# Optimization experiments

Hardware: AMD Instinct MI355X
Metric: run time of the kernel (lower is better)

## Reference

```python
import jax, jax.numpy as jnp
import numpy as np

B, C, H, W = 32, 512, 32, 32
C8 = C // 8


def setup_inputs() -> dict:
    key = jax.random.key(0)
    ks = jax.random.split(key, 4)
    x = jax.random.normal(ks[0], (B, C, W, H), dtype=jnp.float32)
    # 1x1 conv weights == channel-mixing matrices [out_c, in_c]
    Wq = jax.random.normal(ks[1], (C8, C), dtype=jnp.float32) * (1.0 / np.sqrt(C))
    Wk = jax.random.normal(ks[2], (C8, C), dtype=jnp.float32) * (1.0 / np.sqrt(C))
    Wv = jax.random.normal(ks[3], (C, C), dtype=jnp.float32) * (1.0 / np.sqrt(C))
    bq = jnp.zeros((C8,), jnp.float32)
    bk = jnp.zeros((C8,), jnp.float32)
    bv = jnp.zeros((C,), jnp.float32)
    alpha = jnp.float32(1.0)  # nonzero so attention path is exercised
    return {"x": x, "Wq": Wq, "bq": bq, "Wk": Wk, "bk": bk, "Wv": Wv, "bv": bv, "alpha": alpha}


def reference(x, Wq, bq, Wk, bk, Wv, bv, alpha):
    b, c, w, h = x.shape
    n = w * h
    xf = x.reshape(b, c, n)  # [B, C, N]
    # 1x1 convs = per-pixel channel GEMMs
    q = jnp.einsum('oc,bcn->bon', Wq, xf) + bq[None, :, None]  # [B, C8, N]
    k = jnp.einsum('oc,bcn->bon', Wk, xf) + bk[None, :, None]  # [B, C8, N]
    v = jnp.einsum('oc,bcn->bon', Wv, xf) + bv[None, :, None]  # [B, C,  N]
    # energy[b, n, m] = q[:, n] . k[:, m]  (unscaled, full attention)
    energy = jnp.einsum('bcn,bcm->bnm', q, k)  # [B, N, N]
    attention = jax.nn.softmax(energy, axis=-1)
    # out[b, c, n] = sum_m v[b, c, m] * attention[b, n, m]
    out = jnp.einsum('bcm,bnm->bcn', v, attention)
    out = out.reshape(b, c, w, h)
    return alpha * out + x
```

## Files before the change

kernel.cpp:

```cpp
#include <hip/hip_runtime.h>
#include <math.h>

#define B_DIM  32
#define C_DIM  512
#define N_DIM  1024
#define LOG2E  1.44269504088896340736f
#define NEG_BIG (-1.0e30f)

typedef __attribute__((ext_vector_type(8))) __bf16 bf16x8;
typedef __attribute__((ext_vector_type(8))) short short8v;
typedef __attribute__((ext_vector_type(4))) short short4v;
typedef __attribute__((ext_vector_type(4))) float floatx4;

__device__ __forceinline__ unsigned short f2bf(float f) {
    unsigned u = __float_as_uint(f);
    return (unsigned short)((u + 0x7FFFu + ((u >> 16) & 1u)) >> 16);
}
__device__ __forceinline__ float bf2f(unsigned short h) {
    return __uint_as_float(((unsigned)h) << 16);
}
__device__ __forceinline__ floatx4 mfma16(short8v a, short8v b, floatx4 c) {
    return __builtin_amdgcn_mfma_f32_16x16x32_bf16(
        __builtin_bit_cast(bf16x8, a), __builtin_bit_cast(bf16x8, b), c, 0, 0, 0);
}
__device__ __forceinline__ float fin(float v) {
    return (__builtin_fabsf(v) <= 1.0e30f) ? v : 0.0f;
}

#define BAR_LDS()  do {                                            \
    asm volatile("s_waitcnt lgkmcnt(0)" ::: "memory");             \
    __builtin_amdgcn_s_barrier();                                  \
    asm volatile("" ::: "memory");                                 \
} while (0)

__global__ __launch_bounds__(256) void tx2_kernel(
    const float* __restrict__ x,
    unsigned short* __restrict__ xth, unsigned short* __restrict__ xtl)
{
    __shared__ float tile[64][65];
    const int n0 = blockIdx.x * 64, c0 = blockIdx.y * 64, b = blockIdx.z;
    const int t = threadIdx.x;

    #pragma unroll
    for (int p = 0; p < 4; ++p) {
        const int r = (t >> 4) + 16 * p;
        const float4 v = *(const float4*)(x + ((size_t)b*C_DIM + c0 + r)*N_DIM
                                          + n0 + (t & 15)*4);
        tile[r][(t&15)*4+0] = v.x;  tile[r][(t&15)*4+1] = v.y;
        tile[r][(t&15)*4+2] = v.z;  tile[r][(t&15)*4+3] = v.w;
    }
    __syncthreads();
    #pragma unroll
    for (int p = 0; p < 2; ++p) {
        const int rn = (t >> 3) + 32 * p;
        const int c8 = (t & 7) * 8;
        short8v hi, lo;
        #pragma unroll
        for (int j = 0; j < 8; ++j) {
            const float f = tile[c8 + j][rn];
            const unsigned short h = f2bf(f);
            hi[j] = (short)h;
            lo[j] = (short)f2bf(f - bf2f(h));
        }
        const size_t base = ((size_t)b*N_DIM + n0 + rn)*C_DIM + c0 + c8;
        *(short8v*)(xth + base) = hi;
        *(short8v*)(xtl + base) = lo;
    }
}

__global__ __launch_bounds__(256) void qkproj_mfma(
    const unsigned short* __restrict__ xth, const unsigned short* __restrict__ xtl,
    const float* __restrict__ Wq, const float* __restrict__ bq,
    const float* __restrict__ Wk, const float* __restrict__ bk,
    unsigned short* __restrict__ qkt)
{
    __shared__ unsigned short Ah[128][40], Al[128][40];
    __shared__ unsigned short Bh[128][40], Bl[128][40];
    const int b = blockIdx.z, n0 = blockIdx.x * 128;
    const int t = threadIdx.x, w = t >> 6, l = t & 63;
    const int la = l & 15, lb = l >> 4;
    const int nh = (w & 1) * 64, oh = (w >> 1) * 64;

    floatx4 acc[4][4];
    #pragma unroll
    for (int i = 0; i < 4; ++i)
        #pragma unroll
        for (int j = 0; j < 4; ++j) acc[i][j] = (floatx4)0.0f;

    for (int k0 = 0; k0 < C_DIM; k0 += 32) {
        #pragma unroll
        for (int p = 0; p < 2; ++p) {
            const int idx = t + 256*p, row = idx >> 2, ch = idx & 3;
            const size_t g = ((size_t)b*N_DIM + n0 + row)*C_DIM + k0 + ch*8;
            *(short8v*)&Ah[row][ch*8] = *(const short8v*)(xth + g);
            *(short8v*)&Al[row][ch*8] = *(const short8v*)(xtl + g);
        }
        #pragma unroll
        for (int p = 0; p < 4; ++p) {
            const int idx = t + 256*p, row = idx >> 3, ch = idx & 7;
            const float* Wrow = (row < 64) ? (Wq + (size_t)row * C_DIM)
                                           : (Wk + (size_t)(row - 64) * C_DIM);
            const float4 wv = *(const float4*)(Wrow + k0 + ch*4);
            const float fv[4] = {wv.x, wv.y, wv.z, wv.w};
            short4v sh, sl;
            #pragma unroll
            for (int j = 0; j < 4; ++j) {
                const unsigned short h = f2bf(fv[j]);
                sh[j] = (short)h;
                sl[j] = (short)f2bf(fv[j] - bf2f(h));
            }
            *(short4v*)&Bh[row][ch*4] = sh;
            *(short4v*)&Bl[row][ch*4] = sl;
        }
        __syncthreads();

        short8v ahf[4], alf[4], bhf[4], blf[4];
        #pragma unroll
        for (int nt = 0; nt < 4; ++nt) {
            ahf[nt] = *(const short8v*)&Ah[nh + nt*16 + la][lb*8];
            alf[nt] = *(const short8v*)&Al[nh + nt*16 + la][lb*8];
        }
        #pragma unroll
        for (int ot = 0; ot < 4; ++ot) {
            bhf[ot] = *(const short8v*)&Bh[oh + ot*16 + la][lb*8];
            blf[ot] = *(const short8v*)&Bl[oh + ot*16 + la][lb*8];
        }
        #pragma unroll
        for (int nt = 0; nt < 4; ++nt)
            #pragma unroll
            for (int ot = 0; ot < 4; ++ot) {
                acc[nt][ot] = mfma16(ahf[nt], bhf[ot], acc[nt][ot]);
                acc[nt][ot] = mfma16(ahf[nt], blf[ot], acc[nt][ot]);
                acc[nt][ot] = mfma16(alf[nt], bhf[ot], acc[nt][ot]);
            }
        __syncthreads();
    }

    const int plane = (oh == 0) ? 0 : 2;
    #pragma unroll
    for (int ot = 0; ot < 4; ++ot) {
        const int o = oh + ot*16 + la;
        const int c = o & 63;
        const float bias = (oh == 0) ? bq[o] : bk[o - 64];
        #pragma unroll
        for (int nt = 0; nt < 4; ++nt)
            #pragma unroll
            for (int r = 0; r < 4; ++r) {
                const int n = n0 + nh + nt*16 + lb*4 + r;
                const float f = acc[nt][ot][r] + bias;
                const unsigned short h = f2bf(f);
                const unsigned short lo16 = f2bf(f - bf2f(h));
                qkt[(((size_t)b*4 + plane    )*N_DIM + n)*64 + c] = h;
                qkt[(((size_t)b*4 + plane + 1)*N_DIM + n)*64 + c] = lo16;
            }
    }
}

__global__ __launch_bounds__(256) void vproj_mfma(
    const unsigned short* __restrict__ xt,
    const float* __restrict__ Wv, const float* __restrict__ bvv,
    unsigned short* __restrict__ vbf)
{
    __shared__ unsigned short Axs[128][40];
    __shared__ unsigned short Bws[128][40];
    const int b = blockIdx.z, m0 = blockIdx.x * 128, c0 = blockIdx.y * 128;
    const int t = threadIdx.x, w = t >> 6, l = t & 63;
    const int la = l & 15, lb = l >> 4;
    const int mh = (w & 1) * 64, chh = (w >> 1) * 64;

    floatx4 acc[4][4];
    #pragma unroll
    for (int i = 0; i < 4; ++i)
        #pragma unroll
        for (int j = 0; j < 4; ++j) acc[i][j] = (floatx4)0.0f;

    for (int k0 = 0; k0 < C_DIM; k0 += 32) {
        #pragma unroll
        for (int p = 0; p < 2; ++p) {
            const int idx = t + 256 * p;
            const int row = idx >> 2, ch = idx & 3;
            *(short8v*)&Axs[row][ch*8] =
                *(const short8v*)(xt + ((size_t)b*N_DIM + m0 + row)*C_DIM + k0 + ch*8);
        }
        #pragma unroll
        for (int p = 0; p < 4; ++p) {
            const int idx = t + 256 * p;
            const int row = idx >> 3, ch = idx & 7;
            const float4 wv = *(const float4*)(Wv + (size_t)(c0 + row)*C_DIM + k0 + ch*4);
            short4v s;
            s[0] = (short)f2bf(wv.x); s[1] = (short)f2bf(wv.y);
            s[2] = (short)f2bf(wv.z); s[3] = (short)f2bf(wv.w);
            *(short4v*)&Bws[row][ch*4] = s;
        }
        __syncthreads();
        short8v af[4], bfv[4];
        #pragma unroll
        for (int mt = 0; mt < 4; ++mt)
            af[mt] = *(const short8v*)&Axs[mh + mt*16 + la][lb*8];
        #pragma unroll
        for (int ct = 0; ct < 4; ++ct)
            bfv[ct] = *(const short8v*)&Bws[chh + ct*16 + la][lb*8];
        #pragma unroll
        for (int mt = 0; mt < 4; ++mt)
            #pragma unroll
            for (int ct = 0; ct < 4; ++ct)
                acc[mt][ct] = mfma16(af[mt], bfv[ct], acc[mt][ct]);
        __syncthreads();
    }
    #pragma unroll
    for (int ct = 0; ct < 4; ++ct) {
        const int c = c0 + chh + ct*16 + la;
        const float bias = bvv[c];
        #pragma unroll
        for (int mt = 0; mt < 4; ++mt) {
            const int m = m0 + mh + mt*16 + lb*4;
            short4v s;
            #pragma unroll
            for (int r = 0; r < 4; ++r) s[r] = (short)f2bf(acc[mt][ct][r] + bias);
            *(short4v*)(vbf + ((size_t)b*C_DIM + c)*N_DIM + m) = s;
        }
    }
}

__global__ __launch_bounds__(256, 2) void attn_mfma(
    const unsigned short* __restrict__ qkt,
    const unsigned short* __restrict__ vbf,
    const float* __restrict__ x,
    const float* __restrict__ alpha_p,
    float* __restrict__ out)
{
    __shared__ unsigned short Qh[32][72], Ql[32][72];
    __shared__ unsigned short Kh[64][72], Kl[64][72];
    __shared__ __align__(16) float S[32][68];
    __shared__ unsigned short Pb[32][72];
    __shared__ float row_m[32], row_l[32], row_scale[32];

    const int id  = blockIdx.x;
    const int lin = (id & 7) * 128 + (id >> 3);
    const int b   = lin >> 5;
    const int n0  = (lin & 31) * 32;

    const int t = threadIdx.x, w = t >> 6, l = t & 63;
    const int la = l & 15, lb = l >> 4;
    const unsigned short* qkb = qkt + (size_t)b * 4 * N_DIM * 64;

    #pragma unroll
    for (int plane = 0; plane < 2; ++plane) {
        const int row = t >> 3;
        const int ch  = t & 7;
        const short8v g = *(const short8v*)(qkb + ((size_t)plane*N_DIM + n0 + row)*64 + ch*8);
        if (plane == 0) *(short8v*)&Qh[row][ch*8] = g;
        else            *(short8v*)&Ql[row][ch*8] = g;
    }
    #pragma unroll
    for (int pp = 0; pp < 4; ++pp) {
        const int plane = pp >> 1;
        const int idx   = t + 256 * (pp & 1);
        const int row   = idx >> 3;
        const int ch    = idx & 7;
        const short8v g = *(const short8v*)(qkb + ((size_t)(2 + plane)*N_DIM + row)*64 + ch*8);
        if (plane == 0) *(short8v*)&Kh[row][ch*8] = g;
        else            *(short8v*)&Kl[row][ch*8] = g;
    }
    if (t < 32) { row_m[t] = NEG_BIG; row_l[t] = 0.0f; row_scale[t] = 1.0f; }
    __syncthreads();

    floatx4 acc[2][8];
    #pragma unroll
    for (int i = 0; i < 2; ++i)
        #pragma unroll
        for (int j = 0; j < 8; ++j) acc[i][j] = (floatx4)0.0f;

    #pragma unroll 1
    for (int it = 0; it < 16; ++it) {
        const int m0  = it * 64;
        const int m0n = (it < 15) ? (m0 + 64) : 0;

        short8v vreg[2][8];
        #pragma unroll
        for (int ks = 0; ks < 2; ++ks) {
            const unsigned short* vp =
                vbf + ((size_t)b*C_DIM + w*128 + la)*N_DIM + m0 + ks*32 + lb*8;
            #pragma unroll
            for (int ct = 0; ct < 8; ++ct)
                vreg[ks][ct] = *(const short8v*)(vp + (size_t)ct*16*N_DIM);
        }
        short8v kreg[4];
        #pragma unroll
        for (int pp = 0; pp < 4; ++pp) {
            const int plane = pp >> 1;
            const int idx   = t + 256 * (pp & 1);
            const int row   = idx >> 3;
            const int ch    = idx & 7;
            kreg[pp] = *(const short8v*)(qkb + ((size_t)(2 + plane)*N_DIM + m0n + row)*64 + ch*8);
        }

        {
            floatx4 e[2] = { (floatx4)0.0f, (floatx4)0.0f };
            #pragma unroll
            for (int ks = 0; ks < 2; ++ks) {
                const short8v ah = *(const short8v*)&Kh[w*16 + la][ks*32 + lb*8];
                const short8v al = *(const short8v*)&Kl[w*16 + la][ks*32 + lb*8];
                #pragma unroll
                for (int nt = 0; nt < 2; ++nt) {
                    const short8v bh = *(const short8v*)&Qh[nt*16 + la][ks*32 + lb*8];
                    const short8v bl = *(const short8v*)&Ql[nt*16 + la][ks*32 + lb*8];
                    e[nt] = mfma16(ah, bh, e[nt]);
                    e[nt] = mfma16(ah, bl, e[nt]);
                    e[nt] = mfma16(al, bh, e[nt]);
                }
            }
            #pragma unroll
            for (int nt = 0; nt < 2; ++nt) {
                floatx4 ev = e[nt];
                #pragma unroll
                for (int r = 0; r < 4; ++r) ev[r] = fin(ev[r]);
                *(floatx4*)&S[nt*16 + la][w*16 + lb*4] = ev;
            }
        }
        BAR_LDS();

        {
            const int row = t >> 3, seg = t & 7;
            const float4 sa = *(const float4*)&S[row][seg*8];
            const float4 sb = *(const float4*)&S[row][seg*8 + 4];
            float mx = fmaxf(fmaxf(fmaxf(sa.x,sa.y), fmaxf(sa.z,sa.w)),
                             fmaxf(fmaxf(sb.x,sb.y), fmaxf(sb.z,sb.w)));
            mx = fmaxf(mx, __shfl_xor(mx, 1));
            mx = fmaxf(mx, __shfl_xor(mx, 2));
            mx = fmaxf(mx, __shfl_xor(mx, 4));
            const float m_old = row_m[row];
            const float m_new = fmaxf(m_old, mx);
            const float p0 = exp2f((sa.x - m_new) * LOG2E);
            const float p1 = exp2f((sa.y - m_new) * LOG2E);
            const float p2 = exp2f((sa.z - m_new) * LOG2E);
            const float p3 = exp2f((sa.w - m_new) * LOG2E);
            const float p4 = exp2f((sb.x - m_new) * LOG2E);
            const float p5 = exp2f((sb.y - m_new) * LOG2E);
            const float p6 = exp2f((sb.z - m_new) * LOG2E);
            const float p7 = exp2f((sb.w - m_new) * LOG2E);
            float sum = ((p0+p1)+(p2+p3)) + ((p4+p5)+(p6+p7));
            sum += __shfl_xor(sum, 1);
            sum += __shfl_xor(sum, 2);
            sum += __shfl_xor(sum, 4);
            short8v pk;
            pk[0]=(short)f2bf(p0); pk[1]=(short)f2bf(p1);
            pk[2]=(short)f2bf(p2); pk[3]=(short)f2bf(p3);
            pk[4]=(short)f2bf(p4); pk[5]=(short)f2bf(p5);
            pk[6]=(short)f2bf(p6); pk[7]=(short)f2bf(p7);
            *(short8v*)&Pb[row][seg*8] = pk;
            if (seg == 0) {
                const float sc = exp2f((m_old - m_new) * LOG2E);
                row_scale[row] = sc;
                row_l[row] = row_l[row] * sc + sum;
                row_m[row] = m_new;
            }
        }
        BAR_LDS();

        {
            float fsc[2][4];
            #pragma unroll
            for (int nt = 0; nt < 2; ++nt)
                #pragma unroll
                for (int r = 0; r < 4; ++r) fsc[nt][r] = row_scale[nt*16 + lb*4 + r];
            #pragma unroll
            for (int nt = 0; nt < 2; ++nt)
                #pragma unroll
                for (int ct = 0; ct < 8; ++ct)
                    #pragma unroll
                    for (int r = 0; r < 4; ++r) acc[nt][ct][r] *= fsc[nt][r];
        }
        #pragma unroll
        for (int ks = 0; ks < 2; ++ks) {
            const short8v pa0 = *(const short8v*)&Pb[la][ks*32 + lb*8];
            const short8v pa1 = *(const short8v*)&Pb[16 + la][ks*32 + lb*8];
            #pragma unroll
            for (int ct = 0; ct < 8; ++ct) {
                acc[0][ct] = mfma16(pa0, vreg[ks][ct], acc[0][ct]);
                acc[1][ct] = mfma16(pa1, vreg[ks][ct], acc[1][ct]);
            }
        }
        BAR_LDS();

        #pragma unroll
        for (int pp = 0; pp < 4; ++pp) {
            const int plane = pp >> 1;
            const int idx   = t + 256 * (pp & 1);
            const int row   = idx >> 3;
            const int ch    = idx & 7;
            if (plane == 0) *(short8v*)&Kh[row][ch*8] = kreg[pp];
            else            *(short8v*)&Kl[row][ch*8] = kreg[pp];
        }
        BAR_LDS();
    }

    const float alpha = alpha_p[0];
    float invl[2][4];
    #pragma unroll
    for (int nt = 0; nt < 2; ++nt)
        #pragma unroll
        for (int r = 0; r < 4; ++r)
            invl[nt][r] = alpha / fmaxf(row_l[nt*16 + lb*4 + r], 1.0e-20f);
    #pragma unroll
    for (int nt = 0; nt < 2; ++nt)
        #pragma unroll
        for (int ct = 0; ct < 8; ++ct) {
            const int c = w*128 + ct*16 + la;
            const size_t base = ((size_t)b*C_DIM + c)*N_DIM + n0 + nt*16 + lb*4;
            const float4 xa = *(const float4*)&x[base];
            float4 o;
            o.x = fmaf(fin(acc[nt][ct][0]), invl[nt][0], xa.x);
            o.y = fmaf(fin(acc[nt][ct][1]), invl[nt][1], xa.y);
            o.z = fmaf(fin(acc[nt][ct][2]), invl[nt][2], xa.z);
            o.w = fmaf(fin(acc[nt][ct][3]), invl[nt][3], xa.w);
            *(float4*)&out[base] = o;
        }
}

extern "C" void kernel_launch(void* const* d_in, const int* in_sizes, int n_in,
                              void* d_out, int out_size, void* d_ws, size_t ws_size,
                              hipStream_t stream)
{
    const float* x     = (const float*)d_in[0];
    const float* Wq    = (const float*)d_in[1];
    const float* bq    = (const float*)d_in[2];
    const float* Wk    = (const float*)d_in[3];
    const float* bk    = (const float*)d_in[4];
    const float* Wv    = (const float*)d_in[5];
    const float* bv    = (const float*)d_in[6];
    const float* alpha = (const float*)d_in[7];
    float* out = (float*)d_out;

    unsigned short* xth = (unsigned short*)d_ws;
    unsigned short* xtl = (unsigned short*)((char*)d_ws + ((size_t)32 << 20));
    unsigned short* vbf = xtl;
    unsigned short* qkt = (unsigned short*)((char*)d_ws + ((size_t)64 << 20));

    tx2_kernel <<<dim3(16, 8, B_DIM), 256, 0, stream>>>(x, xth, xtl);
    qkproj_mfma<<<dim3(8, 1, B_DIM), 256, 0, stream>>>(xth, xtl, Wq, bq, Wk, bk, qkt);
    vproj_mfma <<<dim3(8, 4, B_DIM), 256, 0, stream>>>(xth, Wv, bv, vbf);
    attn_mfma  <<<dim3(B_DIM * 32), 256, 0, stream>>>(qkt, vbf, x, alpha, out);
}
```

Baseline: 371.0 us.

## Precompute bf16 weights once and double attention query tile to 64 rows

A new prep kernel converts Wq/Wk (hi/lo split) and Wv to bf16 once, staging them in the output buffer before attention overwrites it, so the projection kernels load bf16 directly instead of reconverting fp32 weights in every block. The attention kernel now processes 64 query rows per block instead of 32, halving the grid and doubling reuse of each streamed K/V tile. It also moves the next-K LDS store earlier, after the S barrier, which removes two barriers per iteration. The cost is more registers (acc grows to 4x8) and LDS per block, which may lower occupancy.

After: 403.5 us. 1.09x slower.

```diff
diff --git a/kernel.cpp b/kernel.cpp
--- a/kernel.cpp
+++ b/kernel.cpp
@@ -32,6 +32,39 @@
     __builtin_amdgcn_s_barrier();                                  \
     asm volatile("" ::: "memory");                                 \
 } while (0)
+
+__global__ __launch_bounds__(256) void wprep_kernel(
+    const float* __restrict__ Wq, const float* __restrict__ Wk,
+    const float* __restrict__ Wv,
+    unsigned short* __restrict__ Wqkh, unsigned short* __restrict__ Wqkl,
+    unsigned short* __restrict__ Wvb)
+{
+    const int r = blockIdx.x;
+    const int t = threadIdx.x;
+    if (t >= 128) return;
+    if (r < 128) {
+        const float* src = (r < 64) ? (Wq + (size_t)r * C_DIM)
+                                    : (Wk + (size_t)(r - 64) * C_DIM);
+        const float4 v = ((const float4*)src)[t];
+        const float fv[4] = {v.x, v.y, v.z, v.w};
+        short4v sh, sl;
+        #pragma unroll
+        for (int j = 0; j < 4; ++j) {
+            const unsigned short h = f2bf(fv[j]);
+            sh[j] = (short)h;
+            sl[j] = (short)f2bf(fv[j] - bf2f(h));
+        }
+        *(short4v*)(Wqkh + (size_t)r * C_DIM + t*4) = sh;
+        *(short4v*)(Wqkl + (size_t)r * C_DIM + t*4) = sl;
+    } else {
+        const int rv = r - 128;
+        const float4 v = ((const float4*)(Wv + (size_t)rv * C_DIM))[t];
+        short4v s;
+        s[0] = (short)f2bf(v.x); s[1] = (short)f2bf(v.y);
+        s[2] = (short)f2bf(v.z); s[3] = (short)f2bf(v.w);
+        *(short4v*)(Wvb + (size_t)rv * C_DIM + t*4) = s;
+    }
+}
 
 __global__ __launch_bounds__(256) void tx2_kernel(
     const float* __restrict__ x,
@@ -70,8 +103,8 @@
 
 __global__ __launch_bounds__(256) void qkproj_mfma(
     const unsigned short* __restrict__ xth, const unsigned short* __restrict__ xtl,
-    const float* __restrict__ Wq, const float* __restrict__ bq,
-    const float* __restrict__ Wk, const float* __restrict__ bk,
+    const unsigned short* __restrict__ Wqkh, const unsigned short* __restrict__ Wqkl,
+    const float* __restrict__ bq, const float* __restrict__ bk,
     unsigned short* __restrict__ qkt)
 {
     __shared__ unsigned short Ah[128][40], Al[128][40];
@@ -94,23 +127,9 @@
             const size_t g = ((size_t)b*N_DIM + n0 + row)*C_DIM + k0 + ch*8;
             *(short8v*)&Ah[row][ch*8] = *(const short8v*)(xth + g);
             *(short8v*)&Al[row][ch*8] = *(const short8v*)(xtl + g);
-        }
-        #pragma unroll
-        for (int p = 0; p < 4; ++p) {
-            const int idx = t + 256*p, row = idx >> 3, ch = idx & 7;
-            const float* Wrow = (row < 64) ? (Wq + (size_t)row * C_DIM)
-                                           : (Wk + (size_t)(row - 64) * C_DIM);
-            const float4 wv = *(const float4*)(Wrow + k0 + ch*4);
-            const float fv[4] = {wv.x, wv.y, wv.z, wv.w};
-            short4v sh, sl;
-            #pragma unroll
-            for (int j = 0; j < 4; ++j) {
-                const unsigned short h = f2bf(fv[j]);
-                sh[j] = (short)h;
-                sl[j] = (short)f2bf(fv[j] - bf2f(h));
-            }
-            *(short4v*)&Bh[row][ch*4] = sh;
-            *(short4v*)&Bl[row][ch*4] = sl;
+            const size_t gw = (size_t)row*C_DIM + k0 + ch*8;
+            *(short8v*)&Bh[row][ch*8] = *(const short8v*)(Wqkh + gw);
+            *(short8v*)&Bl[row][ch*8] = *(const short8v*)(Wqkl + gw);
         }
         __syncthreads();
 
@@ -158,7 +177,7 @@
 
 __global__ __launch_bounds__(256) void vproj_mfma(
     const unsigned short* __restrict__ xt,
-    const float* __restrict__ Wv, const float* __restrict__ bvv,
+    const unsigned short* __restrict__ Wvb, const float* __restrict__ bvv,
     unsigned short* __restrict__ vbf)
 {
     __shared__ unsigned short Axs[128][40];
@@ -181,16 +200,8 @@
             const int row = idx >> 2, ch = idx & 3;
             *(short8v*)&Axs[row][ch*8] =
                 *(const short8v*)(xt + ((size_t)b*N_DIM + m0 + row)*C_DIM + k0 + ch*8);
-        }
-        #pragma unroll
-        for (int p = 0; p < 4; ++p) {
-            const int idx = t + 256 * p;
-            const int row = idx >> 3, ch = idx & 7;
-            const float4 wv = *(const float4*)(Wv + (size_t)(c0 + row)*C_DIM + k0 + ch*4);
-            short4v s;
-            s[0] = (short)f2bf(wv.x); s[1] = (short)f2bf(wv.y);
-            s[2] = (short)f2bf(wv.z); s[3] = (short)f2bf(wv.w);
-            *(short4v*)&Bws[row][ch*4] = s;
+            *(short8v*)&Bws[row][ch*8] =
+                *(const short8v*)(Wvb + (size_t)(c0 + row)*C_DIM + k0 + ch*8);
         }
         __syncthreads();
         short8v af[4], bfv[4];
@@ -229,45 +240,45 @@
     const float* __restrict__ alpha_p,
     float* __restrict__ out)
 {
-    __shared__ unsigned short Qh[32][72], Ql[32][72];
+    __shared__ unsigned short Qh[64][72], Ql[64][72];
     __shared__ unsigned short Kh[64][72], Kl[64][72];
-    __shared__ __align__(16) float S[32][68];
-    __shared__ unsigned short Pb[32][72];
-    __shared__ float row_m[32], row_l[32], row_scale[32];
+    __shared__ __align__(16) float S[64][68];
+    __shared__ unsigned short Pb[64][72];
+    __shared__ float row_m[64], row_l[64], row_scale[64];
 
     const int id  = blockIdx.x;
-    const int lin = (id & 7) * 128 + (id >> 3);
-    const int b   = lin >> 5;
-    const int n0  = (lin & 31) * 32;
+    const int lin = (id & 7) * 64 + (id >> 3);
+    const int b   = lin >> 4;
+    const int n0  = (lin & 15) * 64;
 
     const int t = threadIdx.x, w = t >> 6, l = t & 63;
     const int la = l & 15, lb = l >> 4;
     const unsigned short* qkb = qkt + (size_t)b * 4 * N_DIM * 64;
 
     #pragma unroll
-    for (int plane = 0; plane < 2; ++plane) {
-        const int row = t >> 3;
-        const int ch  = t & 7;
-        const short8v g = *(const short8v*)(qkb + ((size_t)plane*N_DIM + n0 + row)*64 + ch*8);
-        if (plane == 0) *(short8v*)&Qh[row][ch*8] = g;
-        else            *(short8v*)&Ql[row][ch*8] = g;
-    }
-    #pragma unroll
-    for (int pp = 0; pp < 4; ++pp) {
-        const int plane = pp >> 1;
-        const int idx   = t + 256 * (pp & 1);
-        const int row   = idx >> 3;
-        const int ch    = idx & 7;
-        const short8v g = *(const short8v*)(qkb + ((size_t)(2 + plane)*N_DIM + row)*64 + ch*8);
-        if (plane == 0) *(short8v*)&Kh[row][ch*8] = g;
-        else            *(short8v*)&Kl[row][ch*8] = g;
-    }
-    if (t < 32) { row_m[t] = NEG_BIG; row_l[t] = 0.0f; row_scale[t] = 1.0f; }
+    for (int plane = 0; plane < 2; ++plane)
+        #pragma unroll
+        for (int p = 0; p < 2; ++p) {
+            const int idx = t + 256*p, row = idx >> 3, ch = idx & 7;
+            const short8v g = *(const short8v*)(qkb + ((size_t)plane*N_DIM + n0 + row)*64 + ch*8);
+            if (plane == 0) *(short8v*)&Qh[row][ch*8] = g;
+            else            *(short8v*)&Ql[row][ch*8] = g;
+        }
+    #pragma unroll
+    for (int plane = 0; plane < 2; ++plane)
+        #pragma unroll
+        for (int p = 0; p < 2; ++p) {
+            const int idx = t + 256*p, row = idx >> 3, ch = idx & 7;
+            const short8v g = *(const short8v*)(qkb + ((size_t)(2 + plane)*N_DIM + row)*64 + ch*8);
+            if (plane == 0) *(short8v*)&Kh[row][ch*8] = g;
+            else            *(short8v*)&Kl[row][ch*8] = g;
+        }
+    if (t < 64) { row_m[t] = NEG_BIG; row_l[t] = 0.0f; row_scale[t] = 1.0f; }
     __syncthreads();
 
-    floatx4 acc[2][8];
-    #pragma unroll
-    for (int i = 0; i < 2; ++i)
+    floatx4 acc[4][8];
+    #pragma unroll
+    for (int i = 0; i < 4; ++i)
         #pragma unroll
         for (int j = 0; j < 8; ++j) acc[i][j] = (floatx4)0.0f;
 
@@ -285,24 +296,23 @@
             for (int ct = 0; ct < 8; ++ct)
                 vreg[ks][ct] = *(const short8v*)(vp + (size_t)ct*16*N_DIM);
         }
-        short8v kreg[4];
-        #pragma unroll
-        for (int pp = 0; pp < 4; ++pp) {
-            const int plane = pp >> 1;
-            const int idx   = t + 256 * (pp & 1);
-            const int row   = idx >> 3;
-            const int ch    = idx & 7;
-            kreg[pp] = *(const short8v*)(qkb + ((size_t)(2 + plane)*N_DIM + m0n + row)*64 + ch*8);
-        }
+        short8v kreg[2][2];
+        #pragma unroll
+        for (int plane = 0; plane < 2; ++plane)
+            #pragma unroll
+            for (int p = 0; p < 2; ++p) {
+                const int idx = t + 256*p, row = idx >> 3, ch = idx & 7;
+                kreg[plane][p] = *(const short8v*)(qkb + ((size_t)(2 + plane)*N_DIM + m0n + row)*64 + ch*8);
+            }
 
         {
-            floatx4 e[2] = { (floatx4)0.0f, (floatx4)0.0f };
+            floatx4 e[4] = {(floatx4)0.0f,(floatx4)0.0f,(floatx4)0.0f,(floatx4)0.0f};
             #pragma unroll
             for (int ks = 0; ks < 2; ++ks) {
                 const short8v ah = *(const short8v*)&Kh[w*16 + la][ks*32 + lb*8];
                 const short8v al = *(const short8v*)&Kl[w*16 + la][ks*32 + lb*8];
                 #pragma unroll
-                for (int nt = 0; nt < 2; ++nt) {
+                for (int nt = 0; nt < 4; ++nt) {
                     const short8v bh = *(const short8v*)&Qh[nt*16 + la][ks*32 + lb*8];
                     const short8v bl = *(const short8v*)&Ql[nt*16 + la][ks*32 + lb*8];
                     e[nt] = mfma16(ah, bh, e[nt]);
@@ -311,7 +321,7 @@
                 }
             }
             #pragma unroll
-            for (int nt = 0; nt < 2; ++nt) {
+            for (int nt = 0; nt < 4; ++nt) {
                 floatx4 ev = e[nt];
                 #pragma unroll
                 for (int r = 0; r < 4; ++r) ev[r] = fin(ev[r]);
@@ -320,8 +330,17 @@
         }
         BAR_LDS();
 
-        {
-            const int row = t >> 3, seg = t & 7;
+        #pragma unroll
+        for (int plane = 0; plane < 2; ++plane)
+            #pragma unroll
+            for (int p = 0; p < 2; ++p) {
+                const int idx = t + 256*p, row = idx >> 3, ch = idx & 7;
+                if (plane == 0) *(short8v*)&Kh[row][ch*8] = kreg[plane][p];
+                else            *(short8v*)&Kl[row][ch*8] = kreg[plane][p];
+            }
+        #pragma unroll
+        for (int sp = 0; sp < 2; ++sp) {
+            const int row = (t >> 3) + 32*sp, seg = t & 7;
             const float4 sa = *(const float4*)&S[row][seg*8];
             const float4 sb = *(const float4*)&S[row][seg*8 + 4];
             float mx = fmaxf(fmaxf(fmaxf(sa.x,sa.y), fmaxf(sa.z,sa.w)),
@@ -359,13 +378,13 @@
         BAR_LDS();
 
         {
-            float fsc[2][4];
-            #pragma unroll
-            for (int nt = 0; nt < 2; ++nt)
+            float fsc[4][4];
+            #pragma unroll
+            for (int nt = 0; nt < 4; ++nt)
                 #pragma unroll
                 for (int r = 0; r < 4; ++r) fsc[nt][r] = row_scale[nt*16 + lb*4 + r];
             #pragma unroll
-            for (int nt = 0; nt < 2; ++nt)
+            for (int nt = 0; nt < 4; ++nt)
                 #pragma unroll
                 for (int ct = 0; ct < 8; ++ct)
                     #pragma unroll
@@ -373,37 +392,28 @@
         }
         #pragma unroll
         for (int ks = 0; ks < 2; ++ks) {
-            const short8v pa0 = *(const short8v*)&Pb[la][ks*32 + lb*8];
-            const short8v pa1 = *(const short8v*)&Pb[16 + la][ks*32 + lb*8];
+            short8v pa[4];
+            #pragma unroll
+            for (int nt = 0; nt < 4; ++nt)
+                pa[nt] = *(const short8v*)&Pb[nt*16 + la][ks*32 + lb*8];
             #pragma unroll
             for (int ct = 0; ct < 8; ++ct) {
-                acc[0][ct] = mfma16(pa0, vreg[ks][ct], acc[0][ct]);
-                acc[1][ct] = mfma16(pa1, vreg[ks][ct], acc[1][ct]);
-            }
-        }
-        BAR_LDS();
-
-        #pragma unroll
-        for (int pp = 0; pp < 4; ++pp) {
-            const int plane = pp >> 1;
-            const int idx   = t + 256 * (pp & 1);
-            const int row   = idx >> 3;
-            const int ch    = idx & 7;
-            if (plane == 0) *(short8v*)&Kh[row][ch*8] = kreg[pp];
-            else            *(short8v*)&Kl[row][ch*8] = kreg[pp];
-        }
-        BAR_LDS();
+                #pragma unroll
+                for (int nt = 0; nt < 4; ++nt)
+                    acc[nt][ct] = mfma16(pa[nt], vreg[ks][ct], acc[nt][ct]);
+            }
+        }
     }
 
     const float alpha = alpha_p[0];
-    float invl[2][4];
-    #pragma unroll
-    for (int nt = 0; nt < 2; ++nt)
+    float invl[4][4];
+    #pragma unroll
+    for (int nt = 0; nt < 4; ++nt)
         #pragma unroll
         for (int r = 0; r < 4; ++r)
             invl[nt][r] = alpha / fmaxf(row_l[nt*16 + lb*4 + r], 1.0e-20f);
     #pragma unroll
-    for (int nt = 0; nt < 2; ++nt)
+    for (int nt = 0; nt < 4; ++nt)
         #pragma unroll
         for (int ct = 0; ct < 8; ++ct) {
             const int c = w*128 + ct*16 + la;
@@ -437,8 +447,13 @@
     unsigned short* vbf = xtl;
     unsigned short* qkt = (unsigned short*)((char*)d_ws + ((size_t)64 << 20));
 
-    tx2_kernel <<<dim3(16, 8, B_DIM), 256, 0, stream>>>(x, xth, xtl);
-    qkproj_mfma<<<dim3(8, 1, B_DIM), 256, 0, stream>>>(xth, xtl, Wq, bq, Wk, bk, qkt);
-    vproj_mfma <<<dim3(8, 4, B_DIM), 256, 0, stream>>>(xth, Wv, bv, vbf);
-    attn_mfma  <<<dim3(B_DIM * 32), 256, 0, stream>>>(qkt, vbf, x, alpha, out);
-}
+    unsigned short* Wqkh = (unsigned short*)d_out;
+    unsigned short* Wqkl = Wqkh + (size_t)128 * C_DIM;
+    unsigned short* Wvb  = Wqkl + (size_t)128 * C_DIM;
+
+    wprep_kernel<<<dim3(640), 256, 0, stream>>>(Wq, Wk, Wv, Wqkh, Wqkl, Wvb);
+    tx2_kernel  <<<dim3(16, 8, B_DIM), 256, 0, stream>>>(x, xth, xtl);
+    qkproj_mfma <<<dim3(8, 1, B_DIM), 256, 0, stream>>>(xth, xtl, Wqkh, Wqkl, bq, bk, qkt);
+    vproj_mfma  <<<dim3(8, 4, B_DIM), 256, 0, stream>>>(xth, Wvb, bv, vbf);
+    attn_mfma   <<<dim3(512), 256, 0, stream>>>(qkt, vbf, x, alpha, out);
+}
```

## Precompute bf16 weights once and drop per-iteration barriers in attention K staging

Applied to the files above, without the earlier changes.

Adds a prep kernel that converts Wq/Wk (hi/lo split) and Wv to bf16 once, using the output buffer as scratch, so the projection kernels load bf16 tiles directly instead of reconverting per block. In the attention loop, the next K tile is written to shared memory before the softmax step instead of after the PV MFMAs, removing two barriers per iteration. The K tile row pitch is reduced from 72 to 68, which changes bank mapping and leaves some rows misaligned for 16-byte vector stores.

Result: faster. 360.6 us (-2.8%).

```diff
diff --git a/kernel.cpp b/kernel.cpp
--- a/kernel.cpp
+++ b/kernel.cpp
@@ -32,6 +32,39 @@
     __builtin_amdgcn_s_barrier();                                  \
     asm volatile("" ::: "memory");                                 \
 } while (0)
+
+__global__ __launch_bounds__(256) void wprep_kernel(
+    const float* __restrict__ Wq, const float* __restrict__ Wk,
+    const float* __restrict__ Wv,
+    unsigned short* __restrict__ Wqkh, unsigned short* __restrict__ Wqkl,
+    unsigned short* __restrict__ Wvb)
+{
+    const int r = blockIdx.x;
+    const int t = threadIdx.x;
+    if (t >= 128) return;
+    if (r < 128) {
+        const float* src = (r < 64) ? (Wq + (size_t)r * C_DIM)
+                                    : (Wk + (size_t)(r - 64) * C_DIM);
+        const float4 v = ((const float4*)src)[t];
+        const float fv[4] = {v.x, v.y, v.z, v.w};
+        short4v sh, sl;
+        #pragma unroll
+        for (int j = 0; j < 4; ++j) {
+            const unsigned short h = f2bf(fv[j]);
+            sh[j] = (short)h;
+            sl[j] = (short)f2bf(fv[j] - bf2f(h));
+        }
+        *(short4v*)(Wqkh + (size_t)r * C_DIM + t*4) = sh;
+        *(short4v*)(Wqkl + (size_t)r * C_DIM + t*4) = sl;
+    } else {
+        const int rv = r - 128;
+        const float4 v = ((const float4*)(Wv + (size_t)rv * C_DIM))[t];
+        short4v s;
+        s[0] = (short)f2bf(v.x); s[1] = (short)f2bf(v.y);
+        s[2] = (short)f2bf(v.z); s[3] = (short)f2bf(v.w);
+        *(short4v*)(Wvb + (size_t)rv * C_DIM + t*4) = s;
+    }
+}
 
 __global__ __launch_bounds__(256) void tx2_kernel(
     const float* __restrict__ x,
@@ -70,8 +103,8 @@
 
 __global__ __launch_bounds__(256) void qkproj_mfma(
     const unsigned short* __restrict__ xth, const unsigned short* __restrict__ xtl,
-    const float* __restrict__ Wq, const float* __restrict__ bq,
-    const float* __restrict__ Wk, const float* __restrict__ bk,
+    const unsigned short* __restrict__ Wqkh, const unsigned short* __restrict__ Wqkl,
+    const float* __restrict__ bq, const float* __restrict__ bk,
     unsigned short* __restrict__ qkt)
 {
     __shared__ unsigned short Ah[128][40], Al[128][40];
@@ -94,23 +127,9 @@
             const size_t g = ((size_t)b*N_DIM + n0 + row)*C_DIM + k0 + ch*8;
             *(short8v*)&Ah[row][ch*8] = *(const short8v*)(xth + g);
             *(short8v*)&Al[row][ch*8] = *(const short8v*)(xtl + g);
-        }
-        #pragma unroll
-        for (int p = 0; p < 4; ++p) {
-            const int idx = t + 256*p, row = idx >> 3, ch = idx & 7;
-            const float* Wrow = (row < 64) ? (Wq + (size_t)row * C_DIM)
-                                           : (Wk + (size_t)(row - 64) * C_DIM);
-            const float4 wv = *(const float4*)(Wrow + k0 + ch*4);
-            const float fv[4] = {wv.x, wv.y, wv.z, wv.w};
-            short4v sh, sl;
-            #pragma unroll
-            for (int j = 0; j < 4; ++j) {
-                const unsigned short h = f2bf(fv[j]);
-                sh[j] = (short)h;
-                sl[j] = (short)f2bf(fv[j] - bf2f(h));
-            }
-            *(short4v*)&Bh[row][ch*4] = sh;
-            *(short4v*)&Bl[row][ch*4] = sl;
+            const size_t gw = (size_t)row*C_DIM + k0 + ch*8;
+            *(short8v*)&Bh[row][ch*8] = *(const short8v*)(Wqkh + gw);
+            *(short8v*)&Bl[row][ch*8] = *(const short8v*)(Wqkl + gw);
         }
         __syncthreads();
 
@@ -158,7 +177,7 @@
 
 __global__ __launch_bounds__(256) void vproj_mfma(
     const unsigned short* __restrict__ xt,
-    const float* __restrict__ Wv, const float* __restrict__ bvv,
+    const unsigned short* __restrict__ Wvb, const float* __restrict__ bvv,
     unsigned short* __restrict__ vbf)
 {
     __shared__ unsigned short Axs[128][40];
@@ -181,16 +200,8 @@
             const int row = idx >> 2, ch = idx & 3;
             *(short8v*)&Axs[row][ch*8] =
                 *(const short8v*)(xt + ((size_t)b*N_DIM + m0 + row)*C_DIM + k0 + ch*8);
-        }
-        #pragma unroll
-        for (int p = 0; p < 4; ++p) {
-            const int idx = t + 256 * p;
-            const int row = idx >> 3, ch = idx & 7;
-            const float4 wv = *(const float4*)(Wv + (size_t)(c0 + row)*C_DIM + k0 + ch*4);
-            short4v s;
-            s[0] = (short)f2bf(wv.x); s[1] = (short)f2bf(wv.y);
-            s[2] = (short)f2bf(wv.z); s[3] = (short)f2bf(wv.w);
-            *(short4v*)&Bws[row][ch*4] = s;
+            *(short8v*)&Bws[row][ch*8] =
+                *(const short8v*)(Wvb + (size_t)(c0 + row)*C_DIM + k0 + ch*8);
         }
         __syncthreads();
         short8v af[4], bfv[4];
@@ -230,7 +241,7 @@
     float* __restrict__ out)
 {
     __shared__ unsigned short Qh[32][72], Ql[32][72];
-    __shared__ unsigned short Kh[64][72], Kl[64][72];
+    __shared__ unsigned short Kh[64][68], Kl[64][68];
     __shared__ __align__(16) float S[32][68];
     __shared__ unsigned short Pb[32][72];
     __shared__ float row_m[32], row_l[32], row_scale[32];
@@ -320,6 +331,15 @@
         }
         BAR_LDS();
 
+        #pragma unroll
+        for (int pp = 0; pp < 4; ++pp) {
+            const int plane = pp >> 1;
+            const int idx   = t + 256 * (pp & 1);
+            const int row   = idx >> 3;
+            const int ch    = idx & 7;
+            if (plane == 0) *(short8v*)&Kh[row][ch*8] = kreg[pp];
+            else            *(short8v*)&Kl[row][ch*8] = kreg[pp];
+        }
         {
             const int row = t >> 3, seg = t & 7;
             const float4 sa = *(const float4*)&S[row][seg*8];
@@ -381,18 +401,6 @@
                 acc[1][ct] = mfma16(pa1, vreg[ks][ct], acc[1][ct]);
             }
         }
-        BAR_LDS();
-
-        #pragma unroll
-        for (int pp = 0; pp < 4; ++pp) {
-            const int plane = pp >> 1;
-            const int idx   = t + 256 * (pp & 1);
-            const int row   = idx >> 3;
-            const int ch    = idx & 7;
-            if (plane == 0) *(short8v*)&Kh[row][ch*8] = kreg[pp];
-            else            *(short8v*)&Kl[row][ch*8] = kreg[pp];
-        }
-        BAR_LDS();
     }
 
     const float alpha = alpha_p[0];
@@ -437,8 +445,13 @@
     unsigned short* vbf = xtl;
     unsigned short* qkt = (unsigned short*)((char*)d_ws + ((size_t)64 << 20));
 
-    tx2_kernel <<<dim3(16, 8, B_DIM), 256, 0, stream>>>(x, xth, xtl);
-    qkproj_mfma<<<dim3(8, 1, B_DIM), 256, 0, stream>>>(xth, xtl, Wq, bq, Wk, bk, qkt);
-    vproj_mfma <<<dim3(8, 4, B_DIM), 256, 0, stream>>>(xth, Wv, bv, vbf);
-    attn_mfma  <<<dim3(B_DIM * 32), 256, 0, stream>>>(qkt, vbf, x, alpha, out);
-}
+    unsigned short* Wqkh = (unsigned short*)d_out;
+    unsigned short* Wqkl = Wqkh + (size_t)128 * C_DIM;
+    unsigned short* Wvb  = Wqkl + (size_t)128 * C_DIM;
+
+    wprep_kernel<<<dim3(640), 256, 0, stream>>>(Wq, Wk, Wv, Wqkh, Wqkl, Wvb);
+    tx2_kernel  <<<dim3(16, 8, B_DIM), 256, 0, stream>>>(x, xth, xtl);
+    qkproj_mfma <<<dim3(8, 1, B_DIM), 256, 0, stream>>>(xth, xtl, Wqkh, Wqkl, bq, bk, qkt);
+    vproj_mfma  <<<dim3(8, 4, B_DIM), 256, 0, stream>>>(xth, Wvb, bv, vbf);
+    attn_mfma   <<<dim3(B_DIM * 32), 256, 0, stream>>>(qkt, vbf, x, alpha, out);
+}
```
